# Optimization experiments

Measured on AMD Instinct MI355X. Metric: run time of the kernel, lower is better.

## Reference

```python
import jax, jax.numpy as jnp
import numpy as np

N = 50000      # nodes
E = 800000     # edges (before self loops)
G = 256        # graphs in batch
N_IN, NHID, HEADS, NOUT = 128, 64, 2, 768
ATT_SLOPE = 0.2   # GATv2 attention LeakyReLU slope (PyG default)
ACT_SLOPE = 0.01  # nn.LeakyReLU default slope


def setup_inputs() -> dict:
    key = jax.random.key(0)
    ks = jax.random.split(key, 20)
    def lin_w(k, fo, fi):
        return (jax.random.normal(k, (fo, fi), jnp.float32) / np.sqrt(fi)).astype(jnp.float32)
    x = jax.random.normal(ks[0], (N, N_IN), jnp.float32)
    edge_index = jax.random.randint(ks[1], (2, E), 0, N, dtype=jnp.int64)
    batch = jnp.sort(jax.random.randint(ks[2], (N,), 0, G, dtype=jnp.int64))
    HC = HEADS * NHID
    return {
        "x": x, "edge_index": edge_index, "batch": batch,
        # conv1: GATv2Conv(N_IN -> NHID, heads=HEADS)
        "w1_l": lin_w(ks[3], HC, N_IN), "b1_l": jnp.zeros((HC,), jnp.float32),
        "w1_r": lin_w(ks[4], HC, N_IN), "b1_r": jnp.zeros((HC,), jnp.float32),
        "att1": jax.random.normal(ks[5], (HEADS, NHID), jnp.float32) / np.sqrt(NHID),
        "bias1": jnp.zeros((HC,), jnp.float32),
        # conv2: GATv2Conv(HC -> NHID, heads=1)
        "w2_l": lin_w(ks[6], NHID, HC), "b2_l": jnp.zeros((NHID,), jnp.float32),
        "w2_r": lin_w(ks[7], NHID, HC), "b2_r": jnp.zeros((NHID,), jnp.float32),
        "att2": jax.random.normal(ks[8], (1, NHID), jnp.float32) / np.sqrt(NHID),
        "bias2": jnp.zeros((NHID,), jnp.float32),
        # MLP head
        "fc1_w": lin_w(ks[9], NHID, NHID), "fc1_b": jnp.zeros((NHID,), jnp.float32),
        "fc2_w": lin_w(ks[10], NOUT, NHID), "fc2_b": jnp.zeros((NOUT,), jnp.float32),
    }


def _leaky(v, slope):
    return jnp.where(v > 0, v, slope * v)


def gatv2_conv(x, src, dst, w_l, b_l, w_r, b_r, att, bias, heads, ch):
    n = x.shape[0]
    xl = (x @ w_l.T + b_l).reshape(n, heads, ch)   # source transform
    xr = (x @ w_r.T + b_r).reshape(n, heads, ch)   # target transform
    m = _leaky(xl[src] + xr[dst], ATT_SLOPE)       # [E, H, C]
    e = jnp.einsum('ehc,hc->eh', m, att)           # attention logits
    # segment softmax over incoming edges of each dst node (self loops guarantee non-empty)
    emax = jax.ops.segment_max(e, dst, num_segments=n)
    ex = jnp.exp(e - emax[dst])
    denom = jax.ops.segment_sum(ex, dst, num_segments=n)
    alpha = ex / denom[dst]
    out = jax.ops.segment_sum(xl[src] * alpha[:, :, None], dst, num_segments=n)
    return out.reshape(n, heads * ch) + bias


def reference(x, edge_index, batch, w1_l, b1_l, w1_r, b1_r, att1, bias1,
              w2_l, b2_l, w2_r, b2_r, att2, bias2, fc1_w, fc1_b, fc2_w, fc2_b):
    loops = jnp.arange(N, dtype=edge_index.dtype)
    src = jnp.concatenate([edge_index[0], loops])  # PyG adds self loops by default
    dst = jnp.concatenate([edge_index[1], loops])
    h = gatv2_conv(x, src, dst, w1_l, b1_l, w1_r, b1_r, att1, bias1, HEADS, NHID)
    h = _leaky(h, ACT_SLOPE)
    h = gatv2_conv(h, src, dst, w2_l, b2_l, w2_r, b2_r, att2, bias2, 1, NHID)
    h = _leaky(h, ACT_SLOPE)
    # global mean pool over graphs
    sums = jax.ops.segment_sum(h, batch, num_segments=G)
    cnt = jax.ops.segment_sum(jnp.ones((N,), h.dtype), batch, num_segments=G)
    pooled = sums / jnp.maximum(cnt, 1.0)[:, None]
    h = _leaky(pooled @ fc1_w.T + fc1_b, ACT_SLOPE)
    return h @ fc2_w.T + fc2_b
```

## Files before the change

### kernel.cpp

```cpp
#include <hip/hip_runtime.h>

#define ATT_SLOPE 0.2f
#define ACT_SLOPE 0.01f

typedef _Float16 half8  __attribute__((ext_vector_type(8)));
typedef _Float16 half2v __attribute__((ext_vector_type(2)));
typedef float    floatx4 __attribute__((ext_vector_type(4)));

#if defined(__has_builtin)
#if __has_builtin(__builtin_amdgcn_fdot2)
#define HAVE_FDOT2 1
#endif
#endif

__device__ __forceinline__ float lrelu(float v, float s) {
    return fmaxf(v, v * s);
}

__device__ __forceinline__ half2v lrelu2(half2v m) {
    half2v t = m * (_Float16)ATT_SLOPE;
    return __builtin_elementwise_max(m, t);
}

__device__ __forceinline__ float dot2(half2v a, half2v b, float c) {
#ifdef HAVE_FDOT2
    return __builtin_amdgcn_fdot2(a, b, c, false);
#else
    return c + (float)a[0] * (float)b[0] + (float)a[1] * (float)b[1];
#endif
}


__global__ __launch_bounds__(256) void k_count_rank(const int* __restrict__ ei, int E, int N,
                                                    int* __restrict__ deg,
                                                    int* __restrict__ rank) {
    int i = blockIdx.x * 256 + threadIdx.x;
    int total = E + N;
    if (i >= total) return;
    int dst = (i < E) ? ei[E + i] : (i - E);
    rank[i] = atomicAdd(&deg[dst], 1);
}

__global__ __launch_bounds__(256) void k_scan_block(const int* __restrict__ deg, int n,
                                                    int* __restrict__ rp1, int* __restrict__ bsum) {
    __shared__ int s[256];
    int tid = threadIdx.x;
    int i = blockIdx.x * 256 + tid;
    s[tid] = (i < n) ? deg[i] : 0;
    __syncthreads();
    for (int off = 1; off < 256; off <<= 1) {
        int t = (tid >= off) ? s[tid - off] : 0;
        __syncthreads();
        s[tid] += t;
        __syncthreads();
    }
    if (i < n) rp1[i] = s[tid];
    if (tid == 255) bsum[blockIdx.x] = s[255];
}

__global__ __launch_bounds__(256) void k_scan_bsum(const int* __restrict__ bsum, int nb,
                                                   int* __restrict__ boff) {
    __shared__ int s[256];
    int tid = threadIdx.x;
    s[tid] = (tid < nb) ? bsum[tid] : 0;
    __syncthreads();
    for (int off = 1; off < 256; off <<= 1) {
        int t = (tid >= off) ? s[tid - off] : 0;
        __syncthreads();
        s[tid] += t;
        __syncthreads();
    }
    if (tid < nb) boff[tid] = (tid > 0) ? s[tid - 1] : 0;
}

__global__ __launch_bounds__(256) void k_scan_add(int* __restrict__ rowptr,
                                                  const int* __restrict__ boff, int n) {
    int i = blockIdx.x * 256 + threadIdx.x;
    if (i < n) rowptr[i + 1] += boff[blockIdx.x];
    if (i == 0) rowptr[0] = 0;
}

__global__ __launch_bounds__(256) void k_scatter(const int* __restrict__ ei, int E, int N,
                                                 const int* __restrict__ rowptr,
                                                 const int* __restrict__ rank,
                                                 int* __restrict__ adj) {
    const int T = E + N;
    const int part = blockIdx.x & 7;
    const int rng = (N + 7) / 8;
    const int lo = part * rng, hi = min(N, lo + rng);
    const int nb = gridDim.x >> 3;
    for (int base = (int)(blockIdx.x >> 3) * 256; base < T; base += nb * 256) {
        int i = base + threadIdx.x;
        if (i >= T) continue;
        int dst = (i < E) ? ei[E + i] : (i - E);
        if (dst >= lo && dst < hi) {
            int src = (i < E) ? ei[i] : dst;
            adj[rowptr[dst] + rank[i]] = src;
        }
    }
}


__global__ __launch_bounds__(256) void k_encode_w(const float* __restrict__ w1l,
                                                  const float* __restrict__ w1r,
                                                  const float* __restrict__ w2l,
                                                  const float* __restrict__ w2r,
                                                  _Float16* __restrict__ W1h,
                                                  _Float16* __restrict__ W1lo,
                                                  _Float16* __restrict__ W2h,
                                                  _Float16* __restrict__ W2lo) {
    int i = blockIdx.x * 256 + threadIdx.x;
    if (i >= 49152) return;
    float v;
    _Float16 *ph, *pl;
    int idx;
    if (i < 32768) {
        idx = i;
        v = (i < 16384) ? w1l[i] : w1r[i - 16384];
        ph = W1h; pl = W1lo;
    } else {
        int j = i - 32768;
        idx = j;
        v = (j < 8192) ? w2l[j] : w2r[j - 8192];
        ph = W2h; pl = W2lo;
    }
    _Float16 h = (_Float16)v;
    ph[idx] = h;
    pl[idx] = (_Float16)(v - (float)h);
}


template <int COUT, bool IN_F32>
__global__ __launch_bounds__(512) void gemm_mfma(const float* __restrict__ Af,
                                                 const _Float16* __restrict__ Ahi,
                                                 const _Float16* __restrict__ Alo, int n_rows,
                                                 const _Float16* __restrict__ Whi,
                                                 const _Float16* __restrict__ Wlo,
                                                 const float* __restrict__ B0,
                                                 const float* __restrict__ B1,
                                                 _Float16* __restrict__ out) {
    constexpr int NT = COUT / 16;
    constexpr int WS = 40;
    __shared__ _Float16 sWh[COUT][WS];
    __shared__ _Float16 sWl[COUT][WS];
    const int tid = threadIdx.x;
    const int lane = tid & 63, wv = tid >> 6;
    const int m = lane & 15, q = lane >> 4;
    const long row0 = ((long)blockIdx.x * 8 + wv) * 16;
    const bool active = row0 < n_rows;
    const long arow = row0 + m;

    floatx4 acc[NT] = {};
    for (int kk = 0; kk < 128; kk += 32) {
        __syncthreads();
        for (int t = tid; t < COUT * 4; t += 512) {
            int c = t >> 2, ch = t & 3;
            *(half8*)&sWh[c][ch * 8] = *(const half8*)&Whi[(size_t)c * 128 + kk + ch * 8];
            *(half8*)&sWl[c][ch * 8] = *(const half8*)&Wlo[(size_t)c * 128 + kk + ch * 8];
        }
        __syncthreads();
        if (active) {
            half8 ah, al;
            if constexpr (IN_F32) {
                float4 a0 = *(const float4*)&Af[(size_t)arow * 128 + kk + q * 8];
                float4 a1 = *(const float4*)&Af[(size_t)arow * 128 + kk + q * 8 + 4];
                float av[8] = {a0.x, a0.y, a0.z, a0.w, a1.x, a1.y, a1.z, a1.w};
                #pragma unroll
                for (int x = 0; x < 8; ++x) {
                    ah[x] = (_Float16)av[x];
                    al[x] = (_Float16)(av[x] - (float)ah[x]);
                }
            } else {
                ah = *(const half8*)&Ahi[(size_t)arow * 128 + kk + q * 8];
                al = *(const half8*)&Alo[(size_t)arow * 128 + kk + q * 8];
            }
            #pragma unroll
            for (int nt = 0; nt < NT; ++nt) {
                half8 bh = *(const half8*)&sWh[nt * 16 + m][q * 8];
                half8 bl = *(const half8*)&sWl[nt * 16 + m][q * 8];
                acc[nt] = __builtin_amdgcn_mfma_f32_16x16x32_f16(ah, bh, acc[nt], 0, 0, 0);
                acc[nt] = __builtin_amdgcn_mfma_f32_16x16x32_f16(al, bh, acc[nt], 0, 0, 0);
                acc[nt] = __builtin_amdgcn_mfma_f32_16x16x32_f16(ah, bl, acc[nt], 0, 0, 0);
            }
        }
    }
    if (active) {
        #pragma unroll
        for (int nt = 0; nt < NT; ++nt) {
            int col = nt * 16 + m;
            float b = (col < COUT / 2) ? B0[col] : B1[col - COUT / 2];
            #pragma unroll
            for (int r = 0; r < 4; ++r) {
                long grow = row0 + q * 4 + r;
                out[(size_t)grow * COUT + col] = (_Float16)(acc[nt][r] + b);
            }
        }
    }
}


__global__ __launch_bounds__(256) void conv1_fused(const _Float16* __restrict__ buf,
                                                   const int* __restrict__ rowptr,
                                                   const int* __restrict__ adj,
                                                   const float* __restrict__ att,
                                                   const float* __restrict__ bias,
                                                   _Float16* __restrict__ h1hi,
                                                   _Float16* __restrict__ h1lo, int n) {
    __shared__ _Float16 sxl[4][16][136];
    __shared__ _Float16 sxr[4][128];
    __shared__ float    sw[4][2][16];
    __shared__ _Float16 satt[128];
    const int tid = threadIdx.x, lane = tid & 63, wv = tid >> 6;
    if (tid < 128) satt[tid] = (_Float16)att[tid];
    __syncthreads();
    int node = blockIdx.x * 4 + wv;
    if (node >= n) return;

    const int jlane = lane & 15;
    const int grp = lane >> 4;
    const int chq = grp * 32;
    const int head = grp >> 1;
    const int wselg = lane >> 5;
    if (lane < 16)
        *(half8*)&sxr[wv][lane * 8] = *(const half8*)&buf[(size_t)node * 256 + 128 + lane * 8];
    asm volatile("s_waitcnt lgkmcnt(0)" ::: "memory");

    const int s = rowptr[node], e = rowptr[node + 1];
    float2 accA = {0.f, 0.f}, accB = {0.f, 0.f};
    float denA = 0.f, denB = 0.f;
    for (int c0 = s; c0 < e; c0 += 16) {
        const int cnt = min(16, e - c0);
        float sacc0 = 0.f, sacc1 = 0.f;
        if (jlane < cnt) {
            int src = adj[c0 + jlane];
            const _Float16* xlp = &buf[(size_t)src * 256 + chq];
            #pragma unroll
            for (int k = 0; k < 4; ++k) {
                half8 l = *(const half8*)&xlp[k * 8];
                half8 r = *(const half8*)&sxr[wv][chq + k * 8];
                half8 a = *(const half8*)&satt[chq + k * 8];
                *(half8*)&sxl[wv][jlane][chq + k * 8] = l;
                float* sp = (k & 1) ? &sacc1 : &sacc0;
                #pragma unroll
                for (int p = 0; p < 4; ++p) {
                    half2v lp = {l[2 * p], l[2 * p + 1]};
                    half2v rp = {r[2 * p], r[2 * p + 1]};
                    half2v ap = {a[2 * p], a[2 * p + 1]};
                    *sp = dot2(lrelu2(lp + rp), ap, *sp);
                }
            }
        }
        float sacc = sacc0 + sacc1;
        float efull = sacc + __shfl_xor(sacc, 16);
        if ((grp & 1) == 0 && jlane < cnt) sw[wv][head][jlane] = __expf(efull);
        asm volatile("s_waitcnt lgkmcnt(0)" ::: "memory");
        int j = 0;
        for (; j + 1 < cnt; j += 2) {
            float w0 = sw[wv][wselg][j], w1 = sw[wv][wselg][j + 1];
            half2v v0 = *(const half2v*)&sxl[wv][j][lane * 2];
            half2v v1 = *(const half2v*)&sxl[wv][j + 1][lane * 2];
            accA.x += w0 * (float)v0[0]; accA.y += w0 * (float)v0[1]; denA += w0;
            accB.x += w1 * (float)v1[0]; accB.y += w1 * (float)v1[1]; denB += w1;
        }
        if (j < cnt) {
            float w0 = sw[wv][wselg][j];
            half2v v0 = *(const half2v*)&sxl[wv][j][lane * 2];
            accA.x += w0 * (float)v0[0]; accA.y += w0 * (float)v0[1]; denA += w0;
        }
        asm volatile("s_waitcnt lgkmcnt(0)" ::: "memory");
    }
    float inv = 1.f / (denA + denB);
    float2 b = *(const float2*)&bias[lane * 2];
    float ox = lrelu((accA.x + accB.x) * inv + b.x, ACT_SLOPE);
    float oy = lrelu((accA.y + accB.y) * inv + b.y, ACT_SLOPE);
    half2v hv, lv;
    hv[0] = (_Float16)ox; lv[0] = (_Float16)(ox - (float)hv[0]);
    hv[1] = (_Float16)oy; lv[1] = (_Float16)(oy - (float)hv[1]);
    *(half2v*)&h1hi[(size_t)node * 128 + lane * 2] = hv;
    *(half2v*)&h1lo[(size_t)node * 128 + lane * 2] = lv;
}


__global__ __launch_bounds__(256) void conv2_fused(const _Float16* __restrict__ buf,
                                                   const int* __restrict__ rowptr,
                                                   const int* __restrict__ adj,
                                                   const float* __restrict__ att,
                                                   const float* __restrict__ bias,
                                                   float* __restrict__ h2, int n) {
    __shared__ _Float16 sxl[4][16][72];
    __shared__ _Float16 sxr[4][64];
    __shared__ float    sw[4][16];
    __shared__ _Float16 satt[64];
    const int tid = threadIdx.x, lane = tid & 63, wv = tid >> 6;
    if (tid < 64) satt[tid] = (_Float16)att[tid];
    __syncthreads();
    int node = blockIdx.x * 4 + wv;
    if (node >= n) return;

    const int jlane = lane & 15;
    const int grp = lane >> 4;
    const int chq = grp * 16;
    if (lane < 8)
        *(half8*)&sxr[wv][lane * 8] = *(const half8*)&buf[(size_t)node * 128 + 64 + lane * 8];
    asm volatile("s_waitcnt lgkmcnt(0)" ::: "memory");

    const int s = rowptr[node], e = rowptr[node + 1];
    float accA = 0.f, accB = 0.f, denA = 0.f, denB = 0.f;
    for (int c0 = s; c0 < e; c0 += 16) {
        const int cnt = min(16, e - c0);
        float sacc = 0.f;
        if (jlane < cnt) {
            int src = adj[c0 + jlane];
            const _Float16* xlp = &buf[(size_t)src * 128 + chq];
            #pragma unroll
            for (int k = 0; k < 2; ++k) {
                half8 l = *(const half8*)&xlp[k * 8];
                half8 r = *(const half8*)&sxr[wv][chq + k * 8];
                half8 a = *(const half8*)&satt[chq + k * 8];
                *(half8*)&sxl[wv][jlane][chq + k * 8] = l;
                #pragma unroll
                for (int p = 0; p < 4; ++p) {
                    half2v lp = {l[2 * p], l[2 * p + 1]};
                    half2v rp = {r[2 * p], r[2 * p + 1]};
                    half2v ap = {a[2 * p], a[2 * p + 1]};
                    sacc = dot2(lrelu2(lp + rp), ap, sacc);
                }
            }
        }
        float s1 = sacc + __shfl_xor(sacc, 16);
        float efull = s1 + __shfl_xor(s1, 32);
        if (grp == 0 && jlane < cnt) sw[wv][jlane] = __expf(efull);
        asm volatile("s_waitcnt lgkmcnt(0)" ::: "memory");
        int j = 0;
        for (; j + 1 < cnt; j += 2) {
            float w0 = sw[wv][j], w1 = sw[wv][j + 1];
            accA += w0 * (float)sxl[wv][j][lane];     denA += w0;
            accB += w1 * (float)sxl[wv][j + 1][lane]; denB += w1;
        }
        if (j < cnt) {
            float w0 = sw[wv][j];
            accA += w0 * (float)sxl[wv][j][lane];
            denA += w0;
        }
        asm volatile("s_waitcnt lgkmcnt(0)" ::: "memory");
    }
    h2[(size_t)node * 64 + lane] = lrelu((accA + accB) / (denA + denB) + bias[lane], ACT_SLOPE);
}


__device__ __forceinline__ int lower_bound(const int* a, int n, int v) {
    int lo = 0, hi = n;
    while (lo < hi) { int mid = (lo + hi) >> 1; if (a[mid] < v) lo = mid + 1; else hi = mid; }
    return lo;
}

__global__ __launch_bounds__(256) void pool_mlp(const float* __restrict__ h2,
                                                const int* __restrict__ batch,
                                                const float* __restrict__ fc1_w,
                                                const float* __restrict__ fc1_b,
                                                const float* __restrict__ fc2_w,
                                                const float* __restrict__ fc2_b,
                                                float* __restrict__ out, int n) {
    const int g = blockIdx.x;
    const int tid = threadIdx.x;
    const int c = tid & 63, q = tid >> 6;
    __shared__ float partial[4][64];
    __shared__ float pooled[64];
    __shared__ float hmid[64];

    int lo = lower_bound(batch, n, g);
    int hi = lower_bound(batch, n, g + 1);

    float sum = 0.f;
    for (int i = lo + q; i < hi; i += 4) sum += h2[(size_t)i * 64 + c];
    partial[q][c] = sum;
    __syncthreads();
    if (q == 0) {
        float s = partial[0][c] + partial[1][c] + partial[2][c] + partial[3][c];
        int cnt = hi - lo;
        pooled[c] = s / (float)max(cnt, 1);
    }
    __syncthreads();
    if (tid < 64) {
        float acc = fc1_b[tid];
        const float* w = &fc1_w[(size_t)tid * 64];
        #pragma unroll
        for (int k = 0; k < 64; ++k) acc += pooled[k] * w[k];
        hmid[tid] = lrelu(acc, ACT_SLOPE);
    }
    __syncthreads();
    for (int o = tid; o < 768; o += 256) {
        float acc = fc2_b[o];
        const float* w = &fc2_w[(size_t)o * 64];
        #pragma unroll
        for (int k = 0; k < 64; ++k) acc += hmid[k] * w[k];
        out[(size_t)g * 768 + o] = acc;
    }
}


extern "C" void kernel_launch(void* const* d_in, const int* in_sizes, int n_in,
                              void* d_out, int out_size, void* d_ws, size_t ws_size,
                              hipStream_t stream) {
    const float* x     = (const float*)d_in[0];
    const int*   ei    = (const int*)d_in[1];
    const int*   batch = (const int*)d_in[2];
    const float* w1_l  = (const float*)d_in[3];
    const float* b1_l  = (const float*)d_in[4];
    const float* w1_r  = (const float*)d_in[5];
    const float* b1_r  = (const float*)d_in[6];
    const float* att1  = (const float*)d_in[7];
    const float* bias1 = (const float*)d_in[8];
    const float* w2_l  = (const float*)d_in[9];
    const float* b2_l  = (const float*)d_in[10];
    const float* w2_r  = (const float*)d_in[11];
    const float* b2_r  = (const float*)d_in[12];
    const float* att2  = (const float*)d_in[13];
    const float* bias2 = (const float*)d_in[14];
    const float* fc1_w = (const float*)d_in[15];
    const float* fc1_b = (const float*)d_in[16];
    const float* fc2_w = (const float*)d_in[17];
    const float* fc2_b = (const float*)d_in[18];
    float* out = (float*)d_out;

    const int N = in_sizes[2];
    const int E = in_sizes[1] / 2;
    const int T = E + N;
    const int G = out_size / 768;

    char* ws = (char*)d_ws;
    size_t off = 0;
    auto alloc = [&](size_t bytes) -> void* {
        void* p = ws + off;
        off = (off + bytes + 255) & ~(size_t)255;
        return p;
    };
    int*      deg    = (int*)alloc((size_t)N * 4);
    int*      rowptr = (int*)alloc((size_t)(N + 1) * 4);
    int*      rank   = (int*)alloc((size_t)T * 4);
    int*      bsum   = (int*)alloc(1024);
    int*      boff   = (int*)alloc(1024);
    int*      adj    = (int*)alloc((size_t)T * 4);
    _Float16* h1hi   = (_Float16*)alloc((size_t)N * 128 * 2);
    _Float16* h1lo   = (_Float16*)alloc((size_t)N * 128 * 2);
    _Float16* W1h    = (_Float16*)alloc(32768 * 2);
    _Float16* W1lo   = (_Float16*)alloc(32768 * 2);
    _Float16* W2h    = (_Float16*)alloc(16384 * 2);
    _Float16* W2lo   = (_Float16*)alloc(16384 * 2);
    _Float16* buf1   = (_Float16*)alloc((size_t)N * 256 * 2);
    _Float16* buf2 = buf1;
    float*    h2   = (float*)((char*)buf1 + (size_t)N * 256);

    const int nbN  = (N + 255) / 256;
    const int nbT  = (T + 255) / 256;
    const int mfmG = (N / 16 + 7) / 8;
    const int edgG = (N + 3) / 4;

    hipMemsetAsync(deg, 0, (size_t)N * 4, stream);
    k_count_rank<<<nbT, 256, 0, stream>>>(ei, E, N, deg, rank);
    k_scan_block<<<nbN, 256, 0, stream>>>(deg, N, rowptr + 1, bsum);
    k_scan_bsum<<<1, 256, 0, stream>>>(bsum, nbN, boff);
    k_scan_add<<<nbN, 256, 0, stream>>>(rowptr, boff, N);
    k_scatter<<<2048, 256, 0, stream>>>(ei, E, N, rowptr, rank, adj);

    k_encode_w<<<192, 256, 0, stream>>>(w1_l, w1_r, w2_l, w2_r, W1h, W1lo, W2h, W2lo);

    gemm_mfma<256, true><<<mfmG, 512, 0, stream>>>(x, nullptr, nullptr, N,
                                                   W1h, W1lo, b1_l, b1_r, buf1);
    conv1_fused<<<edgG, 256, 0, stream>>>(buf1, rowptr, adj, att1, bias1, h1hi, h1lo, N);

    gemm_mfma<128, false><<<mfmG, 512, 0, stream>>>(nullptr, h1hi, h1lo, N,
                                                    W2h, W2lo, b2_l, b2_r, buf2);
    conv2_fused<<<edgG, 256, 0, stream>>>(buf2, rowptr, adj, att2, bias2, h2, N);

    pool_mlp<<<G, 256, 0, stream>>>(h2, batch, fc1_w, fc1_b, fc2_w, fc2_b, out, N);
}
```

Before: 299.6 us.

## Fuse global mean-pool accumulation into conv2 via atomics

conv2 no longer writes per-node h2 to memory. Each output value is atomically added into a per-graph sum buffer, which the weight-encode kernel zeroes. pool_mlp then only scales the precomputed sums by the node count instead of streaming all node features. This drops an N×64 float write and read-back, but adds many contended float atomics on 256×64 addresses and makes the summation order nondeterministic.

```diff
diff --git a/kernel.cpp b/kernel.cpp
--- a/kernel.cpp
+++ b/kernel.cpp
@@ -108,9 +108,14 @@
                                                   _Float16* __restrict__ W1h,
                                                   _Float16* __restrict__ W1lo,
                                                   _Float16* __restrict__ W2h,
-                                                  _Float16* __restrict__ W2lo) {
+                                                  _Float16* __restrict__ W2lo,
+                                                  float* __restrict__ gsum, int gn) {
     int i = blockIdx.x * 256 + threadIdx.x;
-    if (i >= 49152) return;
+    if (i >= 49152 + gn) return;
+    if (i >= 49152) {
+        gsum[i - 49152] = 0.f;
+        return;
+    }
     float v;
     _Float16 *ph, *pl;
     int idx;
@@ -286,7 +291,8 @@
                                                    const int* __restrict__ adj,
                                                    const float* __restrict__ att,
                                                    const float* __restrict__ bias,
-                                                   float* __restrict__ h2, int n) {
+                                                   const int* __restrict__ batch,
+                                                   float* __restrict__ gsum, int n) {
     __shared__ _Float16 sxl[4][16][72];
     __shared__ _Float16 sxr[4][64];
     __shared__ float    sw[4][16];
@@ -344,7 +350,8 @@
         }
         asm volatile("s_waitcnt lgkmcnt(0)" ::: "memory");
     }
-    h2[(size_t)node * 64 + lane] = lrelu((accA + accB) / (denA + denB) + bias[lane], ACT_SLOPE);
+    float val = lrelu((accA + accB) / (denA + denB) + bias[lane], ACT_SLOPE);
+    atomicAdd(&gsum[(size_t)batch[node] * 64 + lane], val);
 }
 
 
@@ -354,7 +361,7 @@
     return lo;
 }
 
-__global__ __launch_bounds__(256) void pool_mlp(const float* __restrict__ h2,
+__global__ __launch_bounds__(256) void pool_mlp(const float* __restrict__ gsum,
                                                 const int* __restrict__ batch,
                                                 const float* __restrict__ fc1_w,
                                                 const float* __restrict__ fc1_b,
@@ -363,23 +370,14 @@
                                                 float* __restrict__ out, int n) {
     const int g = blockIdx.x;
     const int tid = threadIdx.x;
-    const int c = tid & 63, q = tid >> 6;
-    __shared__ float partial[4][64];
     __shared__ float pooled[64];
     __shared__ float hmid[64];
 
     int lo = lower_bound(batch, n, g);
     int hi = lower_bound(batch, n, g + 1);
-
-    float sum = 0.f;
-    for (int i = lo + q; i < hi; i += 4) sum += h2[(size_t)i * 64 + c];
-    partial[q][c] = sum;
-    __syncthreads();
-    if (q == 0) {
-        float s = partial[0][c] + partial[1][c] + partial[2][c] + partial[3][c];
-        int cnt = hi - lo;
-        pooled[c] = s / (float)max(cnt, 1);
-    }
+    float inv = 1.f / (float)max(hi - lo, 1);
+
+    if (tid < 64) pooled[tid] = gsum[(size_t)g * 64 + tid] * inv;
     __syncthreads();
     if (tid < 64) {
         float acc = fc1_b[tid];
@@ -447,14 +445,15 @@
     _Float16* W1lo   = (_Float16*)alloc(32768 * 2);
     _Float16* W2h    = (_Float16*)alloc(16384 * 2);
     _Float16* W2lo   = (_Float16*)alloc(16384 * 2);
+    float*    gsum   = (float*)alloc((size_t)G * 64 * 4);
     _Float16* buf1   = (_Float16*)alloc((size_t)N * 256 * 2);
     _Float16* buf2 = buf1;
-    float*    h2   = (float*)((char*)buf1 + (size_t)N * 256);
 
     const int nbN  = (N + 255) / 256;
     const int nbT  = (T + 255) / 256;
     const int mfmG = (N / 16 + 7) / 8;
     const int edgG = (N + 3) / 4;
+    const int encG = (49152 + G * 64 + 255) / 256;
 
     hipMemsetAsync(deg, 0, (size_t)N * 4, stream);
     k_count_rank<<<nbT, 256, 0, stream>>>(ei, E, N, deg, rank);
@@ -463,7 +462,8 @@
     k_scan_add<<<nbN, 256, 0, stream>>>(rowptr, boff, N);
     k_scatter<<<2048, 256, 0, stream>>>(ei, E, N, rowptr, rank, adj);
 
-    k_encode_w<<<192, 256, 0, stream>>>(w1_l, w1_r, w2_l, w2_r, W1h, W1lo, W2h, W2lo);
+    k_encode_w<<<encG, 256, 0, stream>>>(w1_l, w1_r, w2_l, w2_r,
+                                         W1h, W1lo, W2h, W2lo, gsum, G * 64);
 
     gemm_mfma<256, true><<<mfmG, 512, 0, stream>>>(x, nullptr, nullptr, N,
                                                    W1h, W1lo, b1_l, b1_r, buf1);
@@ -471,7 +471,7 @@
 
     gemm_mfma<128, false><<<mfmG, 512, 0, stream>>>(nullptr, h1hi, h1lo, N,
                                                     W2h, W2lo, b2_l, b2_r, buf2);
-    conv2_fused<<<edgG, 256, 0, stream>>>(buf2, rowptr, adj, att2, bias2, h2, N);
-
-    pool_mlp<<<G, 256, 0, stream>>>(h2, batch, fc1_w, fc1_b, fc2_w, fc2_b, out, N);
-}
+    conv2_fused<<<edgG, 256, 0, stream>>>(buf2, rowptr, adj, att2, bias2, batch, gsum, N);
+
+    pool_mlp<<<G, 256, 0, stream>>>(gsum, batch, fc1_w, fc1_b, fc2_w, fc2_b, out, N);
+}
```

New measurement: 303.0 us. Within noise of the previous version (+1.1%).
